# Optimization experiments

Measured on AMD Instinct MI355X. Metric: run time of the kernel, lower is better.

The kernel has to match this reference:

```python
import jax, jax.numpy as jnp
import numpy as np

B, S, H = 16, 4096, 1024
P = 64            # static max passages per sample (torch computes this at runtime)
TITLE_ID, CTX_ID = 1, 2
NEG_INF = float('-inf')


def setup_inputs() -> dict:
    key = jax.random.key(0)
    k1, k2 = jax.random.split(key)
    outputs = jax.random.normal(k1, (B, S, H), dtype=jnp.float32)
    vt_w = jax.random.normal(k2, (3 * H,), dtype=jnp.float32) * 0.02

    # Build input_ids with ragged per-sample passage structure:
    # <t> title tokens and <c> context tokens at interleaved sorted positions.
    rng = np.random.default_rng(0)
    ids = rng.integers(10, 30000, size=(B, S)).astype(np.int32)
    counts = rng.integers(8, P + 1, size=B)
    counts[0] = P  # ensure runtime max equals static P (matches torch max_)
    for b in range(B):
        n = counts[b]
        pos = np.sort(rng.choice(np.arange(1, S), size=2 * n, replace=False))
        ids[b, pos[0::2]] = TITLE_ID
        ids[b, pos[1::2]] = CTX_ID
    input_ids = jnp.asarray(ids)
    return {"outputs": outputs, "vt_w": vt_w, "input_ids": input_ids,
            "max_passages": P, "title_id": TITLE_ID, "ctx_id": CTX_ID}


def _gather_packed(outputs, input_ids, tok, p):
    """Gather hidden states at positions where input_ids==tok, packed left,
    zero-padded to length p. Returns ([B,p,H] feats, [B,p] valid mask)."""
    mask = input_ids == tok                              # [B,S]
    s = input_ids.shape[1]
    # stable packing: sorted positions of matches first, sentinel s after
    keys = jnp.where(mask, jnp.arange(s)[None, :], s)    # [B,S]
    pos = jnp.sort(keys, axis=-1)[:, :p]                 # [B,p]
    idx = jnp.minimum(pos, s - 1)
    feats = jnp.take_along_axis(outputs, idx[:, :, None], axis=1)  # [B,p,H]
    valid = pos < s                                      # [B,p]
    return feats * valid[:, :, None], valid


def reference(outputs, vt_w, input_ids, max_passages, title_id, ctx_id):
    p = max_passages
    ctx, valid = _gather_packed(outputs, input_ids, ctx_id, p)      # [B,p,H]
    ttl, _ = _gather_packed(outputs, input_ids, title_id, p)        # [B,p,H]
    cls = outputs[:, 0, :][:, None, :] * valid[:, :, None]          # [B,p,H]
    rep = jnp.concatenate([cls, ttl, ctx], axis=-1)                 # [B,p,3H]
    scores = jnp.einsum('bpd,d->bp', rep, vt_w)                     # tiny linear
    return scores + jnp.where(valid, 0.0, NEG_INF)
```

## Files before the change

### kernel.cpp

```cpp
#include <hip/hip_runtime.h>
#include <math.h>

#define B 16
#define S 4096
#define H 1024
#define P 64
#define TITLE_ID 1
#define CTX_ID 2

#define NEG_SENTINEL (-3.0e38f)

#define NPROD B
#define NCONS (B * P)

__global__ __launch_bounds__(256) void fused_kernel(
    const float* __restrict__ outputs,
    const float* __restrict__ w,
    const int*   __restrict__ ids,
    float* __restrict__ out,
    int*   __restrict__ ws)
{
    const int tid = threadIdx.x;
    int* flags = ws + B * 2 * P;

    if (blockIdx.x < NPROD) {
        const int b = blockIdx.x;
        const int* row = ids + b * S;
        constexpr int SEG = S / 256;
        const int base = tid * SEG;

        __shared__ int sc[2][256];
        __shared__ int tpos[P];
        __shared__ int cpos[P];
        if (tid < P) { tpos[tid] = -1; cpos[tid] = -1; }

        int vals[SEG];
        const int4* row4 = (const int4*)(row + base);
        #pragma unroll
        for (int i = 0; i < SEG / 4; ++i) {
            const int4 v = row4[i];
            vals[4*i+0] = v.x; vals[4*i+1] = v.y;
            vals[4*i+2] = v.z; vals[4*i+3] = v.w;
        }
        int ct = 0, cc = 0;
        #pragma unroll
        for (int i = 0; i < SEG; ++i) {
            ct += (vals[i] == TITLE_ID);
            cc += (vals[i] == CTX_ID);
        }
        sc[0][tid] = (ct << 16) | cc;
        __syncthreads();

        int src = 0;
        #pragma unroll
        for (int off = 1; off < 256; off <<= 1) {
            int v = sc[src][tid];
            if (tid >= off) v += sc[src][tid - off];
            sc[1 - src][tid] = v;
            src = 1 - src;
            __syncthreads();
        }
        const int incl = sc[src][tid];
        int rt = (incl >> 16) - ct;
        int rc = (incl & 0xffff) - cc;

        #pragma unroll
        for (int i = 0; i < SEG; ++i) {
            if (vals[i] == TITLE_ID) { if (rt < P) tpos[rt] = base + i; ++rt; }
            if (vals[i] == CTX_ID)   { if (rc < P) cpos[rc] = base + i; ++rc; }
        }
        __syncthreads();

        if (tid < P) {
            ws[b * (2 * P) + tid]     = tpos[tid];
            ws[b * (2 * P) + P + tid] = cpos[tid];
        }
        __threadfence();
        __syncthreads();
        if (tid == 0)
            __hip_atomic_store(&flags[b], 1, __ATOMIC_RELEASE,
                               __HIP_MEMORY_SCOPE_AGENT);
    } else {
        const int idx = blockIdx.x - NPROD;
        const int p = idx & (P - 1);
        const int b = idx >> 6;

        const float4* w4 = (const float4*)w;
        const float4 wc = w4[tid];
        const float4 wt = w4[256 + tid];
        const float4 wx = w4[512 + tid];
        const float4 a0 = ((const float4*)(outputs + (size_t)b * S * H))[tid];
        const float cls_dot = a0.x*wc.x + a0.y*wc.y + a0.z*wc.z + a0.w*wc.w;

        __shared__ int s_tp, s_cp;
        if (tid == 0) {
            while (__hip_atomic_load(&flags[b], __ATOMIC_ACQUIRE,
                                     __HIP_MEMORY_SCOPE_AGENT) != 1)
                __builtin_amdgcn_s_sleep(1);
            s_tp = __hip_atomic_load(&ws[b * (2 * P) + p], __ATOMIC_RELAXED,
                                     __HIP_MEMORY_SCOPE_AGENT);
            s_cp = __hip_atomic_load(&ws[b * (2 * P) + P + p], __ATOMIC_RELAXED,
                                     __HIP_MEMORY_SCOPE_AGENT);
        }
        __syncthreads();
        const int tp = s_tp, cp = s_cp;

        float acc = 0.f;
        if (cp >= 0) {
            acc = cls_dot;
            const float4 ax = ((const float4*)(outputs + ((size_t)b * S + cp) * H))[tid];
            acc += ax.x*wx.x + ax.y*wx.y + ax.z*wx.z + ax.w*wx.w;
        }
        if (tp >= 0) {
            const float4 at = ((const float4*)(outputs + ((size_t)b * S + tp) * H))[tid];
            acc += at.x*wt.x + at.y*wt.y + at.z*wt.z + at.w*wt.w;
        }

        #pragma unroll
        for (int off = 32; off > 0; off >>= 1) acc += __shfl_down(acc, off, 64);

        __shared__ float wsum[4];
        if ((tid & 63) == 0) wsum[tid >> 6] = acc;
        __syncthreads();
        if (tid == 0)
            out[b * P + p] = (cp >= 0) ? (wsum[0] + wsum[1] + wsum[2] + wsum[3])
                                       : NEG_SENTINEL;
    }
}

extern "C" void kernel_launch(void* const* d_in, const int* in_sizes, int n_in,
                              void* d_out, int out_size, void* d_ws, size_t ws_size,
                              hipStream_t stream) {
    const float* outputs   = (const float*)d_in[0];
    const float* vt_w      = (const float*)d_in[1];
    const int*   input_ids = (const int*)d_in[2];
    float* out = (float*)d_out;
    int*   ws  = (int*)d_ws;

    fused_kernel<<<NPROD + NCONS, 256, 0, stream>>>(outputs, vt_w, input_ids, out, ws);
}
```

Measured before the change: 344.1 us.

## Replace producer/consumer spin-wait with redundant per-block scan of id row

Removes the producer blocks and the global flag spin-wait. Each consumer block now scans its own sample's id row and finds the p-th title and context positions itself, using a wavefront shuffle scan in place of the shared-memory Hillis-Steele scan. This drops the inter-block synchronization, workspace traffic and the risk of stale flags. The cost is redundant id reads across the 64 blocks of each sample.

```diff
diff --git a/kernel.cpp b/kernel.cpp
--- a/kernel.cpp
+++ b/kernel.cpp
@@ -10,122 +10,100 @@
 
 #define NEG_SENTINEL (-3.0e38f)
 
-#define NPROD B
-#define NCONS (B * P)
-
 __global__ __launch_bounds__(256) void fused_kernel(
     const float* __restrict__ outputs,
     const float* __restrict__ w,
     const int*   __restrict__ ids,
-    float* __restrict__ out,
-    int*   __restrict__ ws)
+    float* __restrict__ out)
 {
-    const int tid = threadIdx.x;
-    int* flags = ws + B * 2 * P;
+    const int tid  = threadIdx.x;
+    const int p    = blockIdx.x & (P - 1);
+    const int b    = blockIdx.x >> 6;
+    const int lane = tid & 63;
+    const int wv   = tid >> 6;
 
-    if (blockIdx.x < NPROD) {
-        const int b = blockIdx.x;
-        const int* row = ids + b * S;
-        constexpr int SEG = S / 256;
-        const int base = tid * SEG;
+    const float4* w4 = (const float4*)w;
+    const float4 wc = w4[tid];
+    const float4 wt = w4[256 + tid];
+    const float4 wx = w4[512 + tid];
+    const float4 a0 = ((const float4*)(outputs + (size_t)b * S * H))[tid];
+    const float cls_dot = a0.x * wc.x + a0.y * wc.y + a0.z * wc.z + a0.w * wc.w;
 
-        __shared__ int sc[2][256];
-        __shared__ int tpos[P];
-        __shared__ int cpos[P];
-        if (tid < P) { tpos[tid] = -1; cpos[tid] = -1; }
-
-        int vals[SEG];
-        const int4* row4 = (const int4*)(row + base);
+    constexpr int SEG = S / 256;
+    const int base = tid * SEG;
+    int vals[SEG];
+    {
+        const int4* row4 = (const int4*)(ids + b * S + base);
         #pragma unroll
         for (int i = 0; i < SEG / 4; ++i) {
             const int4 v = row4[i];
-            vals[4*i+0] = v.x; vals[4*i+1] = v.y;
-            vals[4*i+2] = v.z; vals[4*i+3] = v.w;
+            vals[4 * i + 0] = v.x; vals[4 * i + 1] = v.y;
+            vals[4 * i + 2] = v.z; vals[4 * i + 3] = v.w;
         }
-        int ct = 0, cc = 0;
+    }
+    int ct = 0, cc = 0;
+    #pragma unroll
+    for (int i = 0; i < SEG; ++i) {
+        ct += (vals[i] == TITLE_ID);
+        cc += (vals[i] == CTX_ID);
+    }
+
+    int incl = (ct << 16) | cc;
+    #pragma unroll
+    for (int off = 1; off < 64; off <<= 1) {
+        const int y = __shfl_up(incl, off, 64);
+        if (lane >= off) incl += y;
+    }
+
+    __shared__ int wtot[4];
+    __shared__ int s_tp, s_cp;
+    if (tid == 0) { s_tp = -1; s_cp = -1; }
+    if (lane == 63) wtot[wv] = incl;
+    __syncthreads();
+
+    int wbase = 0;
+    #pragma unroll
+    for (int k = 0; k < 4; ++k) wbase += (k < wv) ? wtot[k] : 0;
+    incl += wbase;
+    const int rt = (incl >> 16) - ct;
+    const int rc = (incl & 0xffff) - cc;
+
+    if ((unsigned)(p - rt) < (unsigned)ct) {
+        int need = p - rt;
         #pragma unroll
-        for (int i = 0; i < SEG; ++i) {
-            ct += (vals[i] == TITLE_ID);
-            cc += (vals[i] == CTX_ID);
-        }
-        sc[0][tid] = (ct << 16) | cc;
-        __syncthreads();
+        for (int i = 0; i < SEG; ++i)
+            if (vals[i] == TITLE_ID) { if (need == 0) s_tp = base + i; --need; }
+    }
+    if ((unsigned)(p - rc) < (unsigned)cc) {
+        int need = p - rc;
+        #pragma unroll
+        for (int i = 0; i < SEG; ++i)
+            if (vals[i] == CTX_ID) { if (need == 0) s_cp = base + i; --need; }
+    }
+    __syncthreads();
+    const int tp = s_tp;
+    const int cp = s_cp;
 
-        int src = 0;
-        #pragma unroll
-        for (int off = 1; off < 256; off <<= 1) {
-            int v = sc[src][tid];
-            if (tid >= off) v += sc[src][tid - off];
-            sc[1 - src][tid] = v;
-            src = 1 - src;
-            __syncthreads();
-        }
-        const int incl = sc[src][tid];
-        int rt = (incl >> 16) - ct;
-        int rc = (incl & 0xffff) - cc;
+    float acc = 0.f;
+    if (cp >= 0) {
+        acc = cls_dot;
+        const float4 ax = ((const float4*)(outputs + ((size_t)b * S + cp) * H))[tid];
+        acc += ax.x * wx.x + ax.y * wx.y + ax.z * wx.z + ax.w * wx.w;
+    }
+    if (tp >= 0) {
+        const float4 at = ((const float4*)(outputs + ((size_t)b * S + tp) * H))[tid];
+        acc += at.x * wt.x + at.y * wt.y + at.z * wt.z + at.w * wt.w;
+    }
 
-        #pragma unroll
-        for (int i = 0; i < SEG; ++i) {
-            if (vals[i] == TITLE_ID) { if (rt < P) tpos[rt] = base + i; ++rt; }
-            if (vals[i] == CTX_ID)   { if (rc < P) cpos[rc] = base + i; ++rc; }
-        }
-        __syncthreads();
+    #pragma unroll
+    for (int off = 32; off > 0; off >>= 1) acc += __shfl_down(acc, off, 64);
 
-        if (tid < P) {
-            ws[b * (2 * P) + tid]     = tpos[tid];
-            ws[b * (2 * P) + P + tid] = cpos[tid];
-        }
-        __threadfence();
-        __syncthreads();
-        if (tid == 0)
-            __hip_atomic_store(&flags[b], 1, __ATOMIC_RELEASE,
-                               __HIP_MEMORY_SCOPE_AGENT);
-    } else {
-        const int idx = blockIdx.x - NPROD;
-        const int p = idx & (P - 1);
-        const int b = idx >> 6;
-
-        const float4* w4 = (const float4*)w;
-        const float4 wc = w4[tid];
-        const float4 wt = w4[256 + tid];
-        const float4 wx = w4[512 + tid];
-        const float4 a0 = ((const float4*)(outputs + (size_t)b * S * H))[tid];
-        const float cls_dot = a0.x*wc.x + a0.y*wc.y + a0.z*wc.z + a0.w*wc.w;
-
-        __shared__ int s_tp, s_cp;
-        if (tid == 0) {
-            while (__hip_atomic_load(&flags[b], __ATOMIC_ACQUIRE,
-                                     __HIP_MEMORY_SCOPE_AGENT) != 1)
-                __builtin_amdgcn_s_sleep(1);
-            s_tp = __hip_atomic_load(&ws[b * (2 * P) + p], __ATOMIC_RELAXED,
-                                     __HIP_MEMORY_SCOPE_AGENT);
-            s_cp = __hip_atomic_load(&ws[b * (2 * P) + P + p], __ATOMIC_RELAXED,
-                                     __HIP_MEMORY_SCOPE_AGENT);
-        }
-        __syncthreads();
-        const int tp = s_tp, cp = s_cp;
-
-        float acc = 0.f;
-        if (cp >= 0) {
-            acc = cls_dot;
-            const float4 ax = ((const float4*)(outputs + ((size_t)b * S + cp) * H))[tid];
-            acc += ax.x*wx.x + ax.y*wx.y + ax.z*wx.z + ax.w*wx.w;
-        }
-        if (tp >= 0) {
-            const float4 at = ((const float4*)(outputs + ((size_t)b * S + tp) * H))[tid];
-            acc += at.x*wt.x + at.y*wt.y + at.z*wt.z + at.w*wt.w;
-        }
-
-        #pragma unroll
-        for (int off = 32; off > 0; off >>= 1) acc += __shfl_down(acc, off, 64);
-
-        __shared__ float wsum[4];
-        if ((tid & 63) == 0) wsum[tid >> 6] = acc;
-        __syncthreads();
-        if (tid == 0)
-            out[b * P + p] = (cp >= 0) ? (wsum[0] + wsum[1] + wsum[2] + wsum[3])
-                                       : NEG_SENTINEL;
-    }
+    __shared__ float wsum[4];
+    if (lane == 0) wsum[wv] = acc;
+    __syncthreads();
+    if (tid == 0)
+        out[b * P + p] = (cp >= 0) ? (wsum[0] + wsum[1] + wsum[2] + wsum[3])
+                                   : NEG_SENTINEL;
 }
 
 extern "C" void kernel_launch(void* const* d_in, const int* in_sizes, int n_in,
@@ -135,7 +113,6 @@
     const float* vt_w      = (const float*)d_in[1];
     const int*   input_ids = (const int*)d_in[2];
     float* out = (float*)d_out;
-    int*   ws  = (int*)d_ws;
 
-    fused_kernel<<<NPROD + NCONS, 256, 0, stream>>>(outputs, vt_w, input_ids, out, ws);
+    fused_kernel<<<B * P, 256, 0, stream>>>(outputs, vt_w, input_ids, out);
 }
```

New measurement: 301.3 us. 12.4% less time.
